# Kernel optimization log

Hardware: AMD Instinct MI355X
Metric: run time of the kernel (lower is better)

The kernel has to match this reference:

```python
import jax, jax.numpy as jnp
import numpy as np

B, T, V, EMB, KBD, H, NF, OUT = 256, 50, 100000, 64, 64, 128, 10, 64


def setup_inputs() -> dict:
    key = jax.random.key(0)
    ks = jax.random.split(key, 18)
    s = 0.05
    f = lambda i, shape: jax.random.normal(ks[i], shape, jnp.float32) * s
    return {
        "X": jax.random.randint(ks[0], (B, T), 0, V),
        "E": f(1, (V, EMB)),
        "KBE": f(2, (V, KBD)),
        "r_matrix": f(3, (NF, KBD)),
        "gru_Wih": f(4, (3 * H, EMB)),
        "gru_Whh": f(5, (3 * H, H)),
        "gru_bih": f(6, (3 * H,)),
        "gru_bhh": f(7, (3 * H,)),
        "u_W": f(8, (KBD, H)),
        "u_b": f(9, (KBD,)),
        "ea_W": f(10, (KBD, KBD)),
        "ea_b": f(11, (KBD,)),
        "u2_W": f(12, (H, KBD + H)),
        "u2_b": f(13, (H,)),
        "m1_W": f(14, (OUT, H)),
        "m1_b": f(15, (OUT,)),
        "m2_W": f(16, (OUT, EMB + KBD)),
        "m2_b": f(17, (OUT,)),
    }


def reference(X, E, KBE, r_matrix, gru_Wih, gru_Whh, gru_bih, gru_bhh,
              u_W, u_b, ea_W, ea_b, u2_W, u2_b, m1_W, m1_b, m2_W, m2_b):
    b, t = X.shape
    nf, d = r_matrix.shape
    hdim = gru_Whh.shape[1]
    # mask row 0 of the embedding tables (padding item)
    Em = E.at[0].set(0.0)
    KBEm = KBE.at[0].set(0.0)
    Sx = Em[X]        # [B,T,EMB]
    KBx = KBEm[X]     # [B,T,KBD]

    h0 = jnp.zeros((b, hdim), Sx.dtype)
    MN0 = jnp.zeros((b, nf, d), Sx.dtype)
    ysum0 = jnp.zeros((b, m1_b.shape[0]), Sx.dtype)

    def step(carry, xs):
        h, MN, ysum = carry
        x_emb, kb = xs
        # torch GRUCell
        gi = x_emb @ gru_Wih.T + gru_bih
        gh = h @ gru_Whh.T + gru_bhh
        ir, iz, inn = jnp.split(gi, 3, axis=1)
        hr, hz, hn = jnp.split(gh, 3, axis=1)
        r = jax.nn.sigmoid(ir + hr)
        z = jax.nn.sigmoid(iz + hz)
        n = jnp.tanh(inn + r * hn)
        h = (1.0 - z) * n + z * h
        # memory write
        EA = jnp.tanh(kb @ ea_W.T + ea_b)[:, None, :] + r_matrix      # [B,NF,D]
        gate = jax.nn.sigmoid(jnp.sum(MN * EA, axis=-1, keepdims=True))  # [B,NF,1]
        MN = MN * (1.0 - gate) + EA * gate
        # memory read
        U = jnp.tanh(h @ u_W.T + u_b)                                  # [B,D]
        AW = jax.nn.softmax(U @ r_matrix.T, axis=1)                    # [B,NF]
        AC = jnp.einsum('bnd,bn->bd', MN, AW)                          # [B,D]
        Ut = jnp.tanh(jnp.concatenate([h, AC], axis=-1) @ u2_W.T + u2_b)
        y = jnp.tanh(Ut @ m1_W.T + m1_b)                               # [B,OUT]
        return (h, MN, ysum + y), None

    (h, MN, ysum), _ = jax.lax.scan(
        step, (h0, MN0, ysum0),
        (Sx.transpose(1, 0, 2), KBx.transpose(1, 0, 2)))
    y = ysum / t

    MergeE = jnp.concatenate([E, KBE], axis=1).at[0].set(0.0)  # [V, EMB+KBD]
    Sy = jnp.tanh(MergeE @ m2_W.T + m2_b)                      # [V, OUT]
    return jax.nn.log_softmax(y @ Sy.T, axis=1)                # [B, V]
```

## Files before the change

kernel.cpp:

```cpp
#include <hip/hip_runtime.h>
#include <hip/hip_bf16.h>
#include <math.h>

#define BB 256
#define TT 50
#define VV 100000
#define EMB 64
#define KBD 64
#define HH 128
#define NF 10
#define OUTD 64
#define G3H 384
#define NTILE 6250
#define DSTR 16
#define NSY 240

typedef __attribute__((ext_vector_type(8))) short sh8;
typedef __attribute__((ext_vector_type(4))) short sh4;
typedef __attribute__((ext_vector_type(4))) float f32x4;

__device__ __forceinline__ float frcp(float x){ return __builtin_amdgcn_rcpf(x); }
__device__ __forceinline__ float sigm(float x){ return frcp(1.0f+__expf(-x)); }
__device__ __forceinline__ float tanhf_(float x){ return 1.0f - 2.0f*frcp(__expf(2.0f*x)+1.0f); }
__device__ __forceinline__ short f2bs(float f){ __hip_bfloat16 h=__float2bfloat16(f); return *reinterpret_cast<short*>(&h); }
__device__ __forceinline__ sh8 ldfrag(const float* p){
  float4 a = *(const float4*)p; float4 b = *(const float4*)(p+4);
  sh8 v;
  v[0]=f2bs(a.x); v[1]=f2bs(a.y); v[2]=f2bs(a.z); v[3]=f2bs(a.w);
  v[4]=f2bs(b.x); v[5]=f2bs(b.y); v[6]=f2bs(b.z); v[7]=f2bs(b.w);
  return v;
}
__device__ __forceinline__ void barrier_lds(){
  asm volatile("s_waitcnt lgkmcnt(0)" ::: "memory");
  __builtin_amdgcn_sched_barrier(0);
  __builtin_amdgcn_s_barrier();
  __builtin_amdgcn_sched_barrier(0);
}

__global__ void k_trans(const float* __restrict__ Wih, const float* __restrict__ eaW,
                        float* __restrict__ WihT, float* __restrict__ eaWT) {
  int stride = gridDim.x*blockDim.x;
  int tid0 = blockIdx.x*blockDim.x + threadIdx.x;
  for (int i=tid0; i<G3H*EMB; i+=stride){ int j=i/EMB, k=i%EMB; WihT[k*G3H+j]=Wih[i]; }
  for (int i=tid0; i<KBD*KBD; i+=stride){ int j=i/KBD, k=i%KBD; eaWT[k*KBD+j]=eaW[i]; }
}

#define PREP 32
__global__ __launch_bounds__(384) void k_pre(
    const int* __restrict__ X, const float* __restrict__ E, const float* __restrict__ KBE,
    const float* __restrict__ WihT, const float* __restrict__ bih, const float* __restrict__ bhh,
    const float* __restrict__ eaWT, const float* __restrict__ eab,
    float* __restrict__ gi_pre, float* __restrict__ ea_pre,
    __hip_bfloat16* __restrict__ ea_bfT) {
  __shared__ float xeL[PREP][EMB];
  __shared__ float kbL[PREP][KBD];
  int tid = threadIdx.x;
  int base = blockIdx.x * PREP;
  for (int i=tid; i<PREP*EMB; i+=384){
    int p=i>>6, k=i&63; int x = X[base+p];
    xeL[p][k] = x ? E[(size_t)x*EMB+k] : 0.0f;
    kbL[p][k] = x ? KBE[(size_t)x*KBD+k] : 0.0f;
  }
  __syncthreads();
  {
    int j = tid;
    float acc[PREP];
    #pragma unroll
    for (int p=0;p<PREP;p++) acc[p]=0.f;
    for (int k=0;k<EMB;k++){
      float w = WihT[k*G3H+j];
      #pragma unroll
      for (int p=0;p<PREP;p++) acc[p] += w*xeL[p][k];
    }
    float bj = bih[j] + (j < 2*HH ? bhh[j] : 0.0f);
    for (int p=0;p<PREP;p++) gi_pre[((size_t)(base+p))*G3H + j] = acc[p]+bj;
  }
  {
    int d = tid & 63; int pg = tid >> 6;
    float bd = eab[d];
    for (int p=pg; p<PREP; p+=6){
      float acc=0.f;
      #pragma unroll 8
      for (int k=0;k<KBD;k++) acc += eaWT[k*KBD+d]*kbL[p][k];
      float v = tanhf(acc + bd);
      int pair = base+p;
      int bb = pair/TT, tt = pair - bb*TT;
      ea_pre[((size_t)pair)*KBD + d] = v;
      ea_bfT[((size_t)bb*64 + d)*64 + tt] = __float2bfloat16(v);
    }
  }
}

__global__ __launch_bounds__(512,2) void k_scanh(
    const float* __restrict__ gi_pre,
    const float* __restrict__ Whh, const float* __restrict__ bhh,
    const float* __restrict__ E, const float* __restrict__ KBE,
    const float* __restrict__ m2W, const float* __restrict__ m2b,
    __hip_bfloat16* __restrict__ Sy,
    __hip_bfloat16* __restrict__ h_stream) {
  __shared__ __hip_bfloat16 hcat[2][16][136];
  const int tid = threadIdx.x;
  const int w = tid>>6, l = tid&63, r16 = l&15, g4 = l>>4;

  if (blockIdx.x >= 16) {
    int kof = g4*8;
    sh8 bbf[4][4];
    float bias[4];
    #pragma unroll
    for (int nt=0;nt<4;nt++){
      int o = nt*16 + r16;
      bias[nt] = m2b[o];
      #pragma unroll
      for (int ks=0;ks<4;ks++) bbf[nt][ks] = ldfrag(m2W + o*128 + ks*32 + kof);
    }
    int wid = (blockIdx.x-16)*8 + w;
    for (int tile=wid; tile<NTILE; tile+=NSY*8){
      int v = tile*16 + r16;
      sh8 aa[4];
      const float* ep = E + (size_t)v*EMB + kof;
      const float* kp = KBE + (size_t)v*KBD + kof;
      aa[0] = ldfrag(ep); aa[1] = ldfrag(ep+32);
      aa[2] = ldfrag(kp); aa[3] = ldfrag(kp+32);
      if (v==0){ sh8 z={0,0,0,0,0,0,0,0}; aa[0]=z;aa[1]=z;aa[2]=z;aa[3]=z; }
      f32x4 acc[4];
      #pragma unroll
      for (int nt=0;nt<4;nt++){ f32x4 z={0.f,0.f,0.f,0.f}; acc[nt]=z; }
      #pragma unroll
      for (int nt=0;nt<4;nt++)
        #pragma unroll
        for (int ks=0;ks<4;ks++)
          acc[nt] = __builtin_amdgcn_mfma_f32_16x16x32_bf16(aa[ks],bbf[nt][ks],acc[nt],0,0,0);
      #pragma unroll
      for (int nt=0;nt<4;nt++){
        #pragma unroll
        for (int r=0;r<4;r++){
          int vv = tile*16 + g4*4 + r;
          Sy[(size_t)vv*OUTD + nt*16 + r16] = __float2bfloat16(tanhf_(acc[nt][r] + bias[nt]));
        }
      }
    }
    return;
  }

  const int b = blockIdx.x;
  const int b0 = b*16;
  for (int i=tid;i<2*16*136;i+=512) ((short*)hcat)[i]=0;

  sh8 whhF[3][4];
  #pragma unroll
  for (int i=0;i<3;i++)
    #pragma unroll
    for (int f=0;f<4;f++)
      whhF[i][f] = ldfrag(Whh + (size_t)((i*8+w)*16 + r16)*HH + f*32 + g4*8);
  float4 bhn = *(const float4*)(bhh + 2*HH + w*16 + g4*4);
  float h_old[4] = {0.f,0.f,0.f,0.f};

  const float* gi_row = gi_pre + (size_t)(b0+r16)*TT*G3H;
  float4 gi0 = *(const float4*)(gi_row + 0*128 + w*16 + g4*4);
  float4 gi1 = *(const float4*)(gi_row + 1*128 + w*16 + g4*4);
  float4 gi2 = *(const float4*)(gi_row + 2*128 + w*16 + g4*4);
  __hip_bfloat16* hsb = h_stream + (size_t)b*TT*16*HH;
  __syncthreads();

  int cur = 0;
  for (int s=0;s<TT;s++){
    int sg = (s+1<TT)? s+1 : TT-1;
    float4 giN0 = *(const float4*)(gi_row + sg*G3H + 0*128 + w*16 + g4*4);
    float4 giN1 = *(const float4*)(gi_row + sg*G3H + 1*128 + w*16 + g4*4);
    float4 giN2 = *(const float4*)(gi_row + sg*G3H + 2*128 + w*16 + g4*4);
    sh8 hb[4];
    #pragma unroll
    for (int f=0;f<4;f++) hb[f] = *(const sh8*)&hcat[cur][r16][f*32+g4*8];
    f32x4 a0={0.f,0.f,0.f,0.f}, a1=a0, a2=a0;
    #pragma unroll
    for (int f=0;f<4;f++){
      a0 = __builtin_amdgcn_mfma_f32_16x16x32_bf16(whhF[0][f], hb[f], a0,0,0,0);
      a1 = __builtin_amdgcn_mfma_f32_16x16x32_bf16(whhF[1][f], hb[f], a1,0,0,0);
      a2 = __builtin_amdgcn_mfma_f32_16x16x32_bf16(whhF[2][f], hb[f], a2,0,0,0);
    }
    sh4 hp;
    #pragma unroll
    for (int r=0;r<4;r++){
      float rr = sigm(gi0[r] + a0[r]);
      float zz = sigm(gi1[r] + a1[r]);
      float nn = tanhf_(gi2[r] + rr*(a2[r] + bhn[r]));
      h_old[r] = (1.f-zz)*nn + zz*h_old[r];
      hp[r] = f2bs(h_old[r]);
    }
    *(sh4*)&hcat[cur^1][r16][w*16+g4*4] = hp;
    *(sh4*)(hsb + ((size_t)s*16 + r16)*HH + w*16 + g4*4) = hp;
    gi0=giN0; gi1=giN1; gi2=giN2;
    barrier_lds();
    cur ^= 1;
  }
}

__global__ __launch_bounds__(512) void k_uaw(
    const __hip_bfloat16* __restrict__ h_stream,
    const float* __restrict__ uW, const float* __restrict__ ub,
    const float* __restrict__ rmat, float* __restrict__ aw_pre) {
  __shared__ __hip_bfloat16 u_sh[8][16][72];
  const int tid = threadIdx.x;
  const int w = tid>>6, l = tid&63, r16 = l&15, g4 = l>>4;
  sh8 uwF[4][4];
  #pragma unroll
  for (int ot=0;ot<4;ot++)
    #pragma unroll
    for (int f=0;f<4;f++)
      uwF[ot][f] = ldfrag(uW + (size_t)(ot*16+r16)*HH + f*32 + g4*8);
  sh8 rmF[2];
  #pragma unroll
  for (int f=0;f<2;f++){
    sh8 z = {0,0,0,0,0,0,0,0};
    if (r16 < NF) z = ldfrag(rmat + (size_t)r16*KBD + f*32 + g4*8);
    rmF[f] = z;
  }
  float4 ubv[4];
  #pragma unroll
  for (int ot=0;ot<4;ot++) ubv[ot] = *(const float4*)(ub + ot*16 + g4*4);

  int p0 = (blockIdx.x*8 + w)*16;
  int t = p0>>8, b0 = p0&255, fb = b0>>4;
  const __hip_bfloat16* hp = h_stream + (size_t)((fb*TT + t)*16)*HH;
  sh8 hb[4];
  #pragma unroll
  for (int f=0;f<4;f++) hb[f] = *(const sh8*)(hp + r16*HH + f*32 + g4*8);
  f32x4 u[4];
  #pragma unroll
  for (int ot=0;ot<4;ot++){ f32x4 z={0.f,0.f,0.f,0.f}; u[ot]=z; }
  #pragma unroll
  for (int ot=0;ot<4;ot++)
    #pragma unroll
    for (int f=0;f<4;f++)
      u[ot] = __builtin_amdgcn_mfma_f32_16x16x32_bf16(uwF[ot][f], hb[f], u[ot],0,0,0);
  #pragma unroll
  for (int ot=0;ot<4;ot++){
    sh4 up;
    #pragma unroll
    for (int r=0;r<4;r++) up[r] = f2bs(tanhf_(u[ot][r] + ubv[ot][r]));
    *(sh4*)&u_sh[w][l&15][ot*16 + g4*4] = up;
  }
  __syncthreads();
  sh8 uf[2];
  #pragma unroll
  for (int f=0;f<2;f++) uf[f] = *(const sh8*)&u_sh[w][r16][f*32 + g4*8];
  f32x4 al={0.f,0.f,0.f,0.f};
  #pragma unroll
  for (int f=0;f<2;f++) al = __builtin_amdgcn_mfma_f32_16x16x32_bf16(rmF[f], uf[f], al,0,0,0);
  float mx = -1e30f;
  #pragma unroll
  for (int r=0;r<4;r++){ if (g4*4+r < NF) mx = fmaxf(mx, al[r]); }
  mx = fmaxf(mx, __shfl_xor(mx,16));
  mx = fmaxf(mx, __shfl_xor(mx,32));
  float av[4]; float ssum=0.f;
  #pragma unroll
  for (int r=0;r<4;r++){ av[r] = (g4*4+r < NF) ? __expf(al[r]-mx) : 0.f; ssum += av[r]; }
  ssum += __shfl_xor(ssum,16); ssum += __shfl_xor(ssum,32);
  float inv = frcp(ssum);
  if (g4<3){
    f32x4 o = {av[0]*inv, av[1]*inv, av[2]*inv, av[3]*inv};
    *(f32x4*)&aw_pre[(size_t)(p0+r16)*16 + g4*4] = o;
  }
}

__global__ __launch_bounds__(512) void k_gram(
    const float* __restrict__ ea_pre, const float* __restrict__ rmat,
    float* __restrict__ Gg, float* __restrict__ Pg) {
  const int tid = threadIdx.x;
  const int w = tid>>6, l = tid&63, r16 = l&15, g4 = l>>4;
  const int b = blockIdx.x*8 + w;
  sh8 aa[4][2];
  #pragma unroll
  for (int i=0;i<4;i++){
    int row = i*16 + r16; if (row > TT-1) row = TT-1;
    #pragma unroll
    for (int f=0;f<2;f++)
      aa[i][f] = ldfrag(ea_pre + ((size_t)b*TT + row)*KBD + f*32 + g4*8);
  }
  sh8 rmB[2];
  #pragma unroll
  for (int f=0;f<2;f++){
    sh8 z = {0,0,0,0,0,0,0,0};
    if (r16 < NF) z = ldfrag(rmat + (size_t)r16*KBD + f*32 + g4*8);
    rmB[f] = z;
  }
  float* Gb = Gg + ((size_t)b<<12);
  #pragma unroll
  for (int i=0;i<4;i++){
    #pragma unroll
    for (int j=0;j<4;j++){
      f32x4 acc={0.f,0.f,0.f,0.f};
      #pragma unroll
      for (int f=0;f<2;f++) acc = __builtin_amdgcn_mfma_f32_16x16x32_bf16(aa[i][f], aa[j][f], acc,0,0,0);
      #pragma unroll
      for (int r=0;r<4;r++) Gb[(i*16+g4*4+r)*64 + j*16+r16] = acc[r];
    }
    f32x4 accp={0.f,0.f,0.f,0.f};
    #pragma unroll
    for (int f=0;f<2;f++) accp = __builtin_amdgcn_mfma_f32_16x16x32_bf16(aa[i][f], rmB[f], accp,0,0,0);
    #pragma unroll
    for (int r=0;r<4;r++) Pg[((size_t)b<<10) + (i*16+g4*4+r)*16 + r16] = accp[r];
  }
}

__global__ __launch_bounds__(640) void k_mnrec(
    const float* __restrict__ Gg, const float* __restrict__ Pg,
    const float* __restrict__ rmat, const float* __restrict__ aw_pre,
    __hip_bfloat16* __restrict__ Aag_bf, __hip_bfloat16* __restrict__ Bag_bf) {
  __shared__ float AagL[TT*52];
  __shared__ float BagL[TT*16];
  const int tid = threadIdx.x;
  const int n = tid>>6, l = tid&63;
  const int b = blockIdx.x;
  for (int i=tid;i<TT*52;i+=640) AagL[i]=0.f;
  for (int i=tid;i<TT*16;i+=640) BagL[i]=0.f;

  float rv = rmat[n*KBD + l];
  float R = rv*rv;
  R += __shfl_xor(R,1); R += __shfl_xor(R,2); R += __shfl_xor(R,4);
  R += __shfl_xor(R,8); R += __shfl_xor(R,16); R += __shfl_xor(R,32);

  float Pn = (l<TT)? Pg[((size_t)b<<10) + l*16 + n] : 0.f;
  const float* Gb = Gg + ((size_t)b<<12);
  float Grow = Gb[l];
  float awt = aw_pre[(size_t)(0*256+b)*16 + n];
  float d=0.f, w=0.f, q=1.f;
  __syncthreads();

  for (int t=0;t<TT;t++){
    int tn = (t+1<TT)? t+1 : TT-1;
    float GrowN = Gb[tn*64 + l];
    float awtN  = aw_pre[(size_t)(tn*256+b)*16 + n];
    float dt = __shfl(d, t);
    float g  = sigm(dt);
    float og = 1.f - g;
    float Pt = __shfl(Pn, t);
    float Ets = Grow + Pt + Pn + R;
    d = og*d + g*Ets;
    w = (l==t)? g : w*og;
    q *= og;
    if (l < TT) atomicAdd(&AagL[t*52 + l], awt*w);
    if (l == 0) BagL[t*16 + n] = awt*(1.f - q);
    Grow = GrowN; awt = awtN;
  }
  __syncthreads();
  for (int i=tid;i<4096;i+=640){
    int row=i>>6, col=i&63;
    float v = (row<TT && col<TT)? AagL[row*52+col] : 0.f;
    Aag_bf[((size_t)b<<12) + i] = __float2bfloat16(v);
  }
  for (int i=tid;i<2048;i+=640){
    int row=i>>5, col=i&31;
    float v = (row<TT && col<NF)? BagL[row*16+col] : 0.f;
    Bag_bf[((size_t)b<<11) + i] = __float2bfloat16(v);
  }
}

__global__ __launch_bounds__(512) void k_ac(
    const __hip_bfloat16* __restrict__ Aag_bf, const __hip_bfloat16* __restrict__ Bag_bf,
    const __hip_bfloat16* __restrict__ ea_bfT, const float* __restrict__ rmat,
    __hip_bfloat16* __restrict__ ac_pre) {
  const int tid = threadIdx.x;
  const int w = tid>>6, l = tid&63, r16 = l&15, g4 = l>>4;
  const int b = blockIdx.x*8 + w;
  sh8 a1[4][2], a2[4];
  #pragma unroll
  for (int i=0;i<4;i++){
    #pragma unroll
    for (int f=0;f<2;f++)
      a1[i][f] = *(const sh8*)(Aag_bf + ((size_t)b<<12) + (i*16+r16)*64 + f*32 + g4*8);
    a2[i] = *(const sh8*)(Bag_bf + ((size_t)b<<11) + (i*16+r16)*32 + g4*8);
  }
  for (int j=0;j<4;j++){
    sh8 bb1[2];
    #pragma unroll
    for (int f=0;f<2;f++)
      bb1[f] = *(const sh8*)(ea_bfT + ((size_t)b<<12) + (j*16+r16)*64 + f*32 + g4*8);
    sh8 bb2;
    #pragma unroll
    for (int c=0;c<8;c++){
      int k = g4*8 + c;
      bb2[c] = (k<NF)? f2bs(rmat[k*KBD + j*16+r16]) : (short)0;
    }
    #pragma unroll
    for (int i=0;i<4;i++){
      f32x4 acc={0.f,0.f,0.f,0.f};
      #pragma unroll
      for (int f=0;f<2;f++) acc = __builtin_amdgcn_mfma_f32_16x16x32_bf16(a1[i][f], bb1[f], acc,0,0,0);
      acc = __builtin_amdgcn_mfma_f32_16x16x32_bf16(a2[i], bb2, acc,0,0,0);
      #pragma unroll
      for (int r=0;r<4;r++){
        int t = i*16 + g4*4 + r;
        if (t < TT)
          ac_pre[((size_t)t*256 + b)*KBD + j*16 + r16] = __float2bfloat16(acc[r]);
      }
    }
  }
}

__global__ __launch_bounds__(512) void k_uty(
    const __hip_bfloat16* __restrict__ h_stream, const __hip_bfloat16* __restrict__ ac_pre,
    const float* __restrict__ u2W, const float* __restrict__ u2b,
    const float* __restrict__ m1W, const float* __restrict__ m1b,
    __hip_bfloat16* __restrict__ y_tmp) {
  __shared__ __hip_bfloat16 ut_sh[16][136];
  const int tid = threadIdx.x;
  const int w = tid>>6, l = tid&63, r16 = l&15, g4 = l>>4;
  const int t = blockIdx.x>>4, btile = blockIdx.x&15;
  const int b0 = btile*16, fb = btile;

  sh8 u2F[6];
  #pragma unroll
  for (int f=0;f<6;f++) u2F[f] = ldfrag(u2W + (size_t)(w*16+r16)*(HH+KBD) + f*32 + g4*8);
  sh8 m1F[4];
  if (w<4){
    #pragma unroll
    for (int f=0;f<4;f++) m1F[f] = ldfrag(m1W + (size_t)(w*16+r16)*HH + f*32 + g4*8);
  }
  float4 u2bv = *(const float4*)(u2b + w*16 + g4*4);

  const __hip_bfloat16* hp = h_stream + (size_t)((fb*TT + t)*16)*HH;
  const __hip_bfloat16* ap = ac_pre + ((size_t)t*256 + b0)*KBD;
  sh8 cb[6];
  #pragma unroll
  for (int f=0;f<4;f++) cb[f] = *(const sh8*)(hp + r16*HH + f*32 + g4*8);
  #pragma unroll
  for (int f=4;f<6;f++) cb[f] = *(const sh8*)(ap + r16*KBD + (f-4)*32 + g4*8);
  f32x4 at={0.f,0.f,0.f,0.f};
  #pragma unroll
  for (int f=0;f<6;f++) at = __builtin_amdgcn_mfma_f32_16x16x32_bf16(u2F[f], cb[f], at,0,0,0);
  sh4 tp;
  #pragma unroll
  for (int r=0;r<4;r++) tp[r] = f2bs(tanhf_(at[r] + u2bv[r]));
  *(sh4*)&ut_sh[r16][w*16+g4*4] = tp;
  __syncthreads();
  if (w<4){
    float4 m1bv = *(const float4*)(m1b + w*16 + g4*4);
    sh8 tb[4];
    #pragma unroll
    for (int f=0;f<4;f++) tb[f] = *(const sh8*)&ut_sh[r16][f*32+g4*8];
    f32x4 ay={0.f,0.f,0.f,0.f};
    #pragma unroll
    for (int f=0;f<4;f++) ay = __builtin_amdgcn_mfma_f32_16x16x32_bf16(m1F[f], tb[f], ay,0,0,0);
    sh4 yp;
    #pragma unroll
    for (int r=0;r<4;r++) yp[r] = f2bs(tanhf_(ay[r] + m1bv[r]));
    *(sh4*)&y_tmp[((size_t)t*256 + b0 + r16)*OUTD + w*16 + g4*4] = yp;
  }
}

__global__ __launch_bounds__(512) void k_fin(
    const __hip_bfloat16* __restrict__ y_tmp, __hip_bfloat16* __restrict__ ybf) {
  int idx = blockIdx.x*512 + threadIdx.x;
  int b = idx>>6, o = idx&63;
  float s = 0.f;
  for (int t=0;t<TT;t++) s += __bfloat162float(y_tmp[((size_t)t*256 + b)*OUTD + o]);
  ybf[(size_t)b*OUTD + o] = __float2bfloat16(s*(1.0f/TT));
}

__global__ __launch_bounds__(256) void k_logits(
    const __hip_bfloat16* __restrict__ ybf, const __hip_bfloat16* __restrict__ Sy,
    float* __restrict__ denom, float* __restrict__ out, int pass) {
  __shared__ float dsum[64];
  int lane = threadIdx.x & 63;
  int w = threadIdx.x >> 6;
  int r16 = lane & 15, g4 = lane >> 4;
  int kof = g4 * 8;
  int tbase = blockIdx.x * 16 + w * 4;
  if (pass==0){
    if (threadIdx.x<64) dsum[threadIdx.x]=0.f;
    __syncthreads();
  }
  sh8 b0[4], b1[4];
  #pragma unroll
  for (int i=0;i<4;i++){
    if (tbase + i < NTILE) {
      const __hip_bfloat16* bp = Sy + ((size_t)((tbase+i)*16 + r16))*OUTD + kof;
      b0[i] = *(const sh8*)bp;
      b1[i] = *(const sh8*)(bp + 32);
    } else {
      sh8 z = {0,0,0,0,0,0,0,0};
      b0[i]=z; b1[i]=z;
    }
  }
  int bg0 = blockIdx.y * 4;
  for (int bgi=0; bgi<4; bgi++){
    int bg = bg0 + bgi;
    const __hip_bfloat16* ap = ybf + (bg*16 + r16)*OUTD + kof;
    sh8 a0 = *(const sh8*)ap;
    sh8 a1 = *(const sh8*)(ap+32);
    if (pass == 0){
      float part[4] = {0.f,0.f,0.f,0.f};
      #pragma unroll
      for (int i=0;i<4;i++){
        if (tbase + i < NTILE){
          f32x4 acc = {0.f,0.f,0.f,0.f};
          acc = __builtin_amdgcn_mfma_f32_16x16x32_bf16(a0,b0[i],acc,0,0,0);
          acc = __builtin_amdgcn_mfma_f32_16x16x32_bf16(a1,b1[i],acc,0,0,0);
          #pragma unroll
          for (int r=0;r<4;r++) part[r] += __expf(acc[r]);
        }
      }
      #pragma unroll
      for (int r=0;r<4;r++){
        float p = part[r];
        p += __shfl_xor(p,1,16); p += __shfl_xor(p,2,16);
        p += __shfl_xor(p,4,16); p += __shfl_xor(p,8,16);
        if (r16==0) atomicAdd(&dsum[bgi*16 + g4*4 + r], p);
      }
    } else {
      float lse[4];
      #pragma unroll
      for (int r=0;r<4;r++) lse[r] = logf(denom[(size_t)(bg*16 + g4*4 + r)*DSTR]);
      #pragma unroll
      for (int i=0;i<4;i++){
        if (tbase + i < NTILE){
          f32x4 acc = {0.f,0.f,0.f,0.f};
          acc = __builtin_amdgcn_mfma_f32_16x16x32_bf16(a0,b0[i],acc,0,0,0);
          acc = __builtin_amdgcn_mfma_f32_16x16x32_bf16(a1,b1[i],acc,0,0,0);
          int vc = (tbase+i)*16 + r16;
          #pragma unroll
          for (int r=0;r<4;r++)
            out[(size_t)(bg*16 + g4*4 + r)*VV + vc] = acc[r] - lse[r];
        }
      }
    }
  }
  if (pass==0){
    __syncthreads();
    if (threadIdx.x<64)
      atomicAdd(&denom[(size_t)(bg0*16 + threadIdx.x)*DSTR], dsum[threadIdx.x]);
  }
}

extern "C" void kernel_launch(void* const* d_in, const int* in_sizes, int n_in,
                              void* d_out, int out_size, void* d_ws, size_t ws_size,
                              hipStream_t stream) {
  const int*   X    = (const int*)  d_in[0];
  const float* E    = (const float*)d_in[1];
  const float* KBE  = (const float*)d_in[2];
  const float* rmat = (const float*)d_in[3];
  const float* Wih  = (const float*)d_in[4];
  const float* Whh  = (const float*)d_in[5];
  const float* bih  = (const float*)d_in[6];
  const float* bhh  = (const float*)d_in[7];
  const float* uW   = (const float*)d_in[8];
  const float* ub   = (const float*)d_in[9];
  const float* eaW  = (const float*)d_in[10];
  const float* eab  = (const float*)d_in[11];
  const float* u2W  = (const float*)d_in[12];
  const float* u2b  = (const float*)d_in[13];
  const float* m1W  = (const float*)d_in[14];
  const float* m1b  = (const float*)d_in[15];
  const float* m2W  = (const float*)d_in[16];
  const float* m2b  = (const float*)d_in[17];
  float* outp = (float*)d_out;

  char* p = (char*)d_ws;
  float* WihT   = (float*)p;            p += (size_t)EMB*G3H*4;
  float* eaWT   = (float*)p;            p += (size_t)KBD*KBD*4;
  float* gi_pre = (float*)p;            p += (size_t)BB*TT*G3H*4;
  float* ea_pre = (float*)p;            p += (size_t)BB*TT*KBD*4;
  float* denom  = (float*)p;            p += (size_t)BB*DSTR*4;
  float* aw_pre = (float*)p;            p += (size_t)BB*TT*16*4;
  float* Gg     = (float*)p;            p += (size_t)BB*64*64*4;
  float* Pg     = (float*)p;            p += (size_t)BB*64*16*4;
  __hip_bfloat16* h_stream = (__hip_bfloat16*)p; p += (size_t)16*TT*16*HH*2;
  __hip_bfloat16* ea_bfT = (__hip_bfloat16*)p;   p += (size_t)BB*64*64*2;
  __hip_bfloat16* Aag_bf = (__hip_bfloat16*)p;   p += (size_t)BB*64*64*2;
  __hip_bfloat16* Bag_bf = (__hip_bfloat16*)p;   p += (size_t)BB*64*32*2;
  __hip_bfloat16* ac_pre = (__hip_bfloat16*)p;   p += (size_t)BB*TT*KBD*2;
  __hip_bfloat16* y_tmp  = (__hip_bfloat16*)p;   p += (size_t)BB*TT*OUTD*2;
  __hip_bfloat16* ybf    = (__hip_bfloat16*)p;   p += (size_t)BB*OUTD*2;
  __hip_bfloat16* Sy     = (__hip_bfloat16*)p;   p += (size_t)VV*OUTD*2;

  k_trans<<<32,256,0,stream>>>(Wih,eaW,WihT,eaWT);
  k_pre<<<(BB*TT)/PREP,384,0,stream>>>(X,E,KBE,WihT,bih,bhh,eaWT,eab,gi_pre,ea_pre,ea_bfT);
  hipMemsetAsync(denom, 0, BB*DSTR*sizeof(float), stream);
  k_scanh<<<256,512,0,stream>>>(gi_pre,Whh,bhh,E,KBE,m2W,m2b,Sy,h_stream);
  k_uaw<<<100,512,0,stream>>>(h_stream,uW,ub,rmat,aw_pre);
  k_gram<<<32,512,0,stream>>>(ea_pre,rmat,Gg,Pg);
  k_mnrec<<<256,640,0,stream>>>(Gg,Pg,rmat,aw_pre,Aag_bf,Bag_bf);
  k_ac<<<32,512,0,stream>>>(Aag_bf,Bag_bf,ea_bfT,rmat,ac_pre);
  k_uty<<<TT*16,512,0,stream>>>(h_stream,ac_pre,u2W,u2b,m1W,m1b,y_tmp);
  k_fin<<<32,512,0,stream>>>(y_tmp,ybf);
  dim3 g1((NTILE + 15)/16, 4, 1);
  k_logits<<<g1,256,0,stream>>>(ybf,Sy,denom,outp,0);
  k_logits<<<g1,256,0,stream>>>(ybf,Sy,denom,outp,1);
}
```

Baseline: 266.0 us.

## Halve active waves in GRU scan, double work per wave, swizzle LDS h buffer

The recurrent GRU scan now uses only 4 of 8 waves, and each active wave computes two 16-column output tiles per gate. The idle waves just match the per-step barriers. The hidden-state LDS buffer loses its padding and uses an XOR swizzle to avoid bank conflicts instead. The step loop is unrolled by two with ping-pong gi prefetch registers. The intent is to lower barrier/synchronisation cost and raise MFMA ILP per wave on the latency-bound serial recurrence, at the cost of higher register pressure and half the wave-level parallelism.

```diff
diff --git a/kernel.cpp b/kernel.cpp
--- a/kernel.cpp
+++ b/kernel.cpp
@@ -98,7 +98,7 @@
     const float* __restrict__ m2W, const float* __restrict__ m2b,
     __hip_bfloat16* __restrict__ Sy,
     __hip_bfloat16* __restrict__ h_stream) {
-  __shared__ __hip_bfloat16 hcat[2][16][136];
+  __shared__ __hip_bfloat16 hcat[2][16][128];
   const int tid = threadIdx.x;
   const int w = tid>>6, l = tid&63, r16 = l&15, g4 = l>>4;
 
@@ -144,54 +144,96 @@
 
   const int b = blockIdx.x;
   const int b0 = b*16;
-  for (int i=tid;i<2*16*136;i+=512) ((short*)hcat)[i]=0;
-
-  sh8 whhF[3][4];
-  #pragma unroll
-  for (int i=0;i<3;i++)
+  for (int i=tid;i<2*16*128;i+=512) ((short*)hcat)[i]=0;
+  __syncthreads();
+  if (w >= 4){
+    for (int s=0;s<TT;s++) barrier_lds();
+    return;
+  }
+  const int swz = (r16&7)<<4;
+
+  sh8 whhF[2][3][4];
+  #pragma unroll
+  for (int t=0;t<2;t++)
+    #pragma unroll
+    for (int g=0;g<3;g++){
+      int chain = (w + 4*t) + 8*g;
+      #pragma unroll
+      for (int f=0;f<4;f++)
+        whhF[t][g][f] = ldfrag(Whh + (size_t)(chain*16 + r16)*HH + f*32 + g4*8);
+    }
+  float4 bhn[2];
+  bhn[0] = *(const float4*)(bhh + 2*HH + w*16 + g4*4);
+  bhn[1] = *(const float4*)(bhh + 2*HH + (w+4)*16 + g4*4);
+  float h_old[2][4] = {{0.f,0.f,0.f,0.f},{0.f,0.f,0.f,0.f}};
+  const float* gi_row = gi_pre + (size_t)(b0+r16)*TT*G3H;
+  __hip_bfloat16* hsb = h_stream + (size_t)b*TT*16*HH;
+
+  int cur = 0;
+  auto stepfn = [&](int s, float4 (&gi)[2][3], int cu){
+    const char* hrow = (const char*)&hcat[cu][r16][0];
+    sh8 hb[4];
     #pragma unroll
     for (int f=0;f<4;f++)
-      whhF[i][f] = ldfrag(Whh + (size_t)((i*8+w)*16 + r16)*HH + f*32 + g4*8);
-  float4 bhn = *(const float4*)(bhh + 2*HH + w*16 + g4*4);
-  float h_old[4] = {0.f,0.f,0.f,0.f};
-
-  const float* gi_row = gi_pre + (size_t)(b0+r16)*TT*G3H;
-  float4 gi0 = *(const float4*)(gi_row + 0*128 + w*16 + g4*4);
-  float4 gi1 = *(const float4*)(gi_row + 1*128 + w*16 + g4*4);
-  float4 gi2 = *(const float4*)(gi_row + 2*128 + w*16 + g4*4);
-  __hip_bfloat16* hsb = h_stream + (size_t)b*TT*16*HH;
-  __syncthreads();
-
-  int cur = 0;
-  for (int s=0;s<TT;s++){
-    int sg = (s+1<TT)? s+1 : TT-1;
-    float4 giN0 = *(const float4*)(gi_row + sg*G3H + 0*128 + w*16 + g4*4);
-    float4 giN1 = *(const float4*)(gi_row + sg*G3H + 1*128 + w*16 + g4*4);
-    float4 giN2 = *(const float4*)(gi_row + sg*G3H + 2*128 + w*16 + g4*4);
-    sh8 hb[4];
-    #pragma unroll
-    for (int f=0;f<4;f++) hb[f] = *(const sh8*)&hcat[cur][r16][f*32+g4*8];
-    f32x4 a0={0.f,0.f,0.f,0.f}, a1=a0, a2=a0;
+      hb[f] = *(const sh8*)(hrow + ((f*64 + g4*16) ^ swz));
+    f32x4 aR[2], aZ[2], aN[2];
+    #pragma unroll
+    for (int t=0;t<2;t++){ f32x4 z={0.f,0.f,0.f,0.f}; aR[t]=z; aZ[t]=z; aN[t]=z; }
     #pragma unroll
     for (int f=0;f<4;f++){
-      a0 = __builtin_amdgcn_mfma_f32_16x16x32_bf16(whhF[0][f], hb[f], a0,0,0,0);
-      a1 = __builtin_amdgcn_mfma_f32_16x16x32_bf16(whhF[1][f], hb[f], a1,0,0,0);
-      a2 = __builtin_amdgcn_mfma_f32_16x16x32_bf16(whhF[2][f], hb[f], a2,0,0,0);
-    }
-    sh4 hp;
-    #pragma unroll
-    for (int r=0;r<4;r++){
-      float rr = sigm(gi0[r] + a0[r]);
-      float zz = sigm(gi1[r] + a1[r]);
-      float nn = tanhf_(gi2[r] + rr*(a2[r] + bhn[r]));
-      h_old[r] = (1.f-zz)*nn + zz*h_old[r];
-      hp[r] = f2bs(h_old[r]);
-    }
-    *(sh4*)&hcat[cur^1][r16][w*16+g4*4] = hp;
-    *(sh4*)(hsb + ((size_t)s*16 + r16)*HH + w*16 + g4*4) = hp;
-    gi0=giN0; gi1=giN1; gi2=giN2;
+      #pragma unroll
+      for (int t=0;t<2;t++){
+        aR[t] = __builtin_amdgcn_mfma_f32_16x16x32_bf16(whhF[t][0][f], hb[f], aR[t],0,0,0);
+        aZ[t] = __builtin_amdgcn_mfma_f32_16x16x32_bf16(whhF[t][1][f], hb[f], aZ[t],0,0,0);
+        aN[t] = __builtin_amdgcn_mfma_f32_16x16x32_bf16(whhF[t][2][f], hb[f], aN[t],0,0,0);
+      }
+    }
+    char* hwrow = (char*)&hcat[cu^1][r16][0];
+    #pragma unroll
+    for (int t=0;t<2;t++){
+      sh4 hp;
+      #pragma unroll
+      for (int r=0;r<4;r++){
+        float rr = sigm(gi[t][0][r] + aR[t][r]);
+        float zz = sigm(gi[t][1][r] + aZ[t][r]);
+        float nn = tanhf_(gi[t][2][r] + rr*(aN[t][r] + bhn[t][r]));
+        h_old[t][r] = (1.f-zz)*nn + zz*h_old[t][r];
+        hp[r] = f2bs(h_old[t][r]);
+      }
+      *(sh4*)(hwrow + (((w+4*t)*32 + g4*8) ^ swz)) = hp;
+      *(sh4*)(hsb + ((size_t)s*16 + r16)*HH + (w+4*t)*16 + g4*4) = hp;
+    }
     barrier_lds();
-    cur ^= 1;
+  };
+
+  float4 gA[2][3], gB[2][3];
+  #pragma unroll
+  for (int t=0;t<2;t++)
+    #pragma unroll
+    for (int g=0;g<3;g++)
+      gA[t][g] = *(const float4*)(gi_row + g*128 + (w+4*t)*16 + g4*4);
+
+  for (int s=0;s<TT;s+=2){
+    {
+      int sg = s+1;
+      #pragma unroll
+      for (int t=0;t<2;t++)
+        #pragma unroll
+        for (int g=0;g<3;g++)
+          gB[t][g] = *(const float4*)(gi_row + (size_t)sg*G3H + g*128 + (w+4*t)*16 + g4*4);
+      stepfn(s, gA, cur);
+      cur ^= 1;
+    }
+    {
+      int sg = (s+2<TT)? s+2 : TT-1;
+      #pragma unroll
+      for (int t=0;t<2;t++)
+        #pragma unroll
+        for (int g=0;g<3;g++)
+          gA[t][g] = *(const float4*)(gi_row + (size_t)sg*G3H + g*128 + (w+4*t)*16 + g4*4);
+      stepfn(s+1, gB, cur);
+      cur ^= 1;
+    }
   }
 }
 
```

New measurement: 260.3 us. 1.02x faster.
